# Kernel optimization log

Measured on AMD Instinct MI355X. Metric: run time of the kernel, lower is better.

The kernel has to match this reference:

```python
import jax, jax.numpy as jnp
import numpy as np

REG_CONST = 0.05  # matches init_kwargs reg_const


def setup_inputs() -> dict:
    key = jax.random.key(0)
    k1, k2, k3 = jax.random.split(key, 3)
    N, D, C = 1_000_000, 128, 10
    X_train = jax.random.normal(k1, (N, D), dtype=jnp.float32)
    y_train = jax.random.randint(k2, (N,), 0, C)
    w = jax.random.normal(k3, (C, D), dtype=jnp.float32) * 0.01
    return {"X_train": X_train, "y_train": y_train, "w": w}


def reference(X_train, y_train, w):
    """Vectorized SVM.calc_gradient: multiclass hinge loss + gradient w.r.t. w.

    Original loops over samples i and classes c:
      margin = scores[c] - scores[y_i] + 1; if margin > 0 (c != y_i):
        loss += margin; grad[y_i] += X[i]; grad[c] -= X[i]
    then loss /= N (+ 0.5*reg*||w||^2), grad /= N (+ reg*w).
    (The original seeds `gradients` with np.random.rand -- a bug; we use the
    intended zero init so the math is deterministic.)
    """
    N = X_train.shape[0]
    C = w.shape[0]
    inv_n = jnp.asarray(1.0 / N, dtype=X_train.dtype)

    scores = X_train @ w.T                                        # [N, C]
    correct = jnp.take_along_axis(scores, y_train[:, None], axis=1)  # [N, 1]
    margins = scores - correct + 1.0                              # [N, C]
    onehot = jax.nn.one_hot(y_train, C, dtype=scores.dtype)       # [N, C]
    mask = jnp.where((margins > 0) & (onehot == 0), 1.0, 0.0).astype(scores.dtype)

    loss = jnp.sum(mask * margins) * inv_n + 0.5 * REG_CONST * jnp.sum(w * w)

    # grad[c] gets -X[i] for each violating (i, c); grad[y_i] gets +X[i] per
    # violating class -> counts[i] copies of X[i] scatter-added to row y_i.
    counts = mask.sum(axis=1)                                     # [N]
    neg_part = mask.T @ X_train                                   # [C, D]
    pos_part = jax.ops.segment_sum(counts[:, None] * X_train, y_train,
                                   num_segments=C)                # [C, D]
    gradients = (pos_part - neg_part) * inv_n + REG_CONST * w
    return gradients, loss
```

## Files before the change

### kernel.cpp

```cpp
#include <hip/hip_runtime.h>

#define REG_CONST 0.05f
#define NCLASS 10
#define DIM 128
#define TILE 64
#define NBLOCKS 768
#define NTHREADS 256

__device__ __forceinline__ void async_ld16(const void* g, void* l) {
  __builtin_amdgcn_global_load_lds(
      (const __attribute__((address_space(1))) void*)g,
      (__attribute__((address_space(3))) void*)l, 16, 0, 0);
}

__global__ __launch_bounds__(NTHREADS, 3)
void svm_fused(const float* __restrict__ X, const int* __restrict__ y,
               const float* __restrict__ w, float* __restrict__ out,
               int ntiles, float inv_n) {
  __shared__ float4 xs[2048];
  __shared__ float4 coefs[192];
  __shared__ float4 wlds4[360];
  __shared__ float  lred[4];

  float* wlds = (float*)wlds4;
  const int t  = threadIdx.x;
  const int l  = t & 63;
  const int wv = t >> 6;

  for (int i = t; i < NCLASS * DIM; i += NTHREADS) {
    int d = i & 127;
    wlds[(i >> 7) * 144 + d + ((d >> 5) << 2)] = w[i];
  }

  const float4* X4 = (const float4*)X;

  const int p1row = (wv << 4) + (l >> 2);
  const int dq    = l & 3;
  const int d4p2 = t & 31;
  const int rg   = t >> 5;

  float4 g[10];
  #pragma unroll
  for (int c = 0; c < 10; ++c) g[c] = make_float4(0.f, 0.f, 0.f, 0.f);
  float loss_acc = 0.f;

  for (int tix = blockIdx.x; tix < ntiles; tix += gridDim.x) {
    const int row0 = tix * TILE;
    __syncthreads();
    #pragma unroll
    for (int ii = 0; ii < 8; ++ii) {
      int i   = (wv << 3) + ii;
      int row = (i << 1) + (l >> 5);
      int d4  = (l & 31) ^ (row & 31);
      async_ld16(X4 + (size_t)(row0 + row) * 32 + d4, xs + (i << 6) + l);
    }
    __syncthreads();

    float s[10];
    #pragma unroll
    for (int c = 0; c < 10; ++c) s[c] = 0.f;
    #pragma unroll
    for (int j = 0; j < 8; ++j) {
      int d4 = (dq << 3) + j;
      float4 x4 = xs[(p1row << 5) + (d4 ^ (p1row & 31))];
      #pragma unroll
      for (int c = 0; c < 10; ++c) {
        float4 w4 = wlds4[c * 36 + dq * 9 + j];
        s[c] = fmaf(x4.x, w4.x, fmaf(x4.y, w4.y,
               fmaf(x4.z, w4.z, fmaf(x4.w, w4.w, s[c]))));
      }
    }
    #pragma unroll
    for (int c = 0; c < 10; ++c) {
      s[c] += __shfl_xor(s[c], 1);
      s[c] += __shfl_xor(s[c], 2);
    }

    int yv = y[row0 + p1row];
    float sy = s[0];
    #pragma unroll
    for (int c = 1; c < 10; ++c) sy = (c == yv) ? s[c] : sy;

    float cnt = 0.f, rl = 0.f;
    float cf[10];
    #pragma unroll
    for (int c = 0; c < 10; ++c) {
      float m = s[c] - sy + 1.0f;
      bool act = (m > 0.f) && (c != yv);
      cf[c] = act ? -1.f : 0.f;
      cnt += act ? 1.f : 0.f;
      rl  += act ? m : 0.f;
    }
    #pragma unroll
    for (int c = 0; c < 10; ++c) cf[c] = (c == yv) ? cnt : cf[c];
    coefs[p1row * 3 + 0] = make_float4(cf[0], cf[1], cf[2], cf[3]);
    coefs[p1row * 3 + 1] = make_float4(cf[4], cf[5], cf[6], cf[7]);
    coefs[p1row * 3 + 2] = make_float4(cf[8], cf[9], 0.f, 0.f);
    if (dq == 0) loss_acc += rl;
    __syncthreads();

    #pragma unroll
    for (int k = 0; k < 8; ++k) {
      int r = (k << 3) + rg;
      float4 x4 = xs[(r << 5) + (d4p2 ^ (r & 31))];
      float4 c0 = coefs[r * 3 + 0];
      float4 c1 = coefs[r * 3 + 1];
      float4 c2 = coefs[r * 3 + 2];
#define ACC4(cc, gi)                         \
      g[gi].x = fmaf(cc, x4.x, g[gi].x);     \
      g[gi].y = fmaf(cc, x4.y, g[gi].y);     \
      g[gi].z = fmaf(cc, x4.z, g[gi].z);     \
      g[gi].w = fmaf(cc, x4.w, g[gi].w);
      ACC4(c0.x, 0) ACC4(c0.y, 1) ACC4(c0.z, 2) ACC4(c0.w, 3)
      ACC4(c1.x, 4) ACC4(c1.y, 5) ACC4(c1.z, 6) ACC4(c1.w, 7)
      ACC4(c2.x, 8) ACC4(c2.y, 9)
#undef ACC4
    }
  }

  float contrib = loss_acc * inv_n;
  if (blockIdx.x == 0) {
    float rw = 0.f;
    for (int i = t; i < NCLASS * DIM; i += NTHREADS) rw = fmaf(w[i], w[i], rw);
    contrib = fmaf(0.5f * REG_CONST, rw, contrib);
  }
  #pragma unroll
  for (int off = 32; off; off >>= 1) contrib += __shfl_down(contrib, off);
  if (l == 0) lred[wv] = contrib;
  __syncthreads();
  if (t == 0) atomicAdd(out + NCLASS * DIM, lred[0] + lred[1] + lred[2] + lred[3]);

  float4* red = xs;
  #pragma unroll
  for (int chunk = 0; chunk < 2; ++chunk) {
    __syncthreads();
    #pragma unroll
    for (int k = 0; k < 5; ++k) red[k * 256 + t] = g[chunk * 5 + k];
    __syncthreads();
    if (t < 160) {
      int k = t >> 5, dd = t & 31;
      float sx = 0.f, syy = 0.f, sz = 0.f, sw = 0.f;
      #pragma unroll
      for (int r8 = 0; r8 < 8; ++r8) {
        float4 v = red[k * 256 + (r8 << 5) + dd];
        sx += v.x; syy += v.y; sz += v.z; sw += v.w;
      }
      int c = chunk * 5 + k;
      int base = c * DIM + (dd << 2);
      float ax = sx * inv_n, ay = syy * inv_n, az = sz * inv_n, aw = sw * inv_n;
      if (blockIdx.x == 0) {
        ax += REG_CONST * w[base + 0];
        ay += REG_CONST * w[base + 1];
        az += REG_CONST * w[base + 2];
        aw += REG_CONST * w[base + 3];
      }
      atomicAdd(out + base + 0, ax);
      atomicAdd(out + base + 1, ay);
      atomicAdd(out + base + 2, az);
      atomicAdd(out + base + 3, aw);
    }
  }
}

extern "C" void kernel_launch(void* const* d_in, const int* in_sizes, int n_in,
                              void* d_out, int out_size, void* d_ws, size_t ws_size,
                              hipStream_t stream) {
  const float* X = (const float*)d_in[0];
  const int*   y = (const int*)d_in[1];
  const float* w = (const float*)d_in[2];
  float* out = (float*)d_out;
  int N = in_sizes[1];
  int ntiles = N / TILE;
  float inv_n = 1.0f / (float)N;
  hipMemsetAsync(d_out, 0, (size_t)out_size * sizeof(float), stream);
  svm_fused<<<NBLOCKS, NTHREADS, 0, stream>>>(X, y, w, out, ntiles, inv_n);
}
```

Baseline: 726.0 us.

## Double-buffer X tiles with async LDS prefetch and keep weights in registers

The kernel now double-buffers X tiles in LDS. It issues the async global-to-LDS load for the next tile before computing on the current one, which removes one block-wide barrier per tile and hides global load latency. The tile shrinks to 32 rows, and the X swizzle is dropped. Class weights now live in registers instead of LDS. Each wave handles its own 8 rows, so the per-row coefficients are shared within a wave without a barrier. The added register pressure (160 weight floats plus 40 accumulators) under launch bounds of 3 blocks per CU may cause spills.

```diff
diff --git a/kernel.cpp b/kernel.cpp
--- a/kernel.cpp
+++ b/kernel.cpp
@@ -3,7 +3,7 @@
 #define REG_CONST 0.05f
 #define NCLASS 10
 #define DIM 128
-#define TILE 64
+#define TILE 32
 #define NBLOCKS 768
 #define NTHREADS 256
 
@@ -17,55 +17,62 @@
 void svm_fused(const float* __restrict__ X, const int* __restrict__ y,
                const float* __restrict__ w, float* __restrict__ out,
                int ntiles, float inv_n) {
-  __shared__ float4 xs[2048];
-  __shared__ float4 coefs[192];
-  __shared__ float4 wlds4[360];
+  __shared__ float4 xs[2][1024];
+  __shared__ float4 coefs[96];
   __shared__ float  lred[4];
 
-  float* wlds = (float*)wlds4;
-  const int t  = threadIdx.x;
-  const int l  = t & 63;
-  const int wv = t >> 6;
+  const int t    = threadIdx.x;
+  const int l    = t & 63;
+  const int wv   = t >> 6;
+  const int dq   = l & 7;
+  const int orow = wv * 8 + (l >> 3);
+  const int d4p  = l & 31;
+  const int h    = l >> 5;
 
-  for (int i = t; i < NCLASS * DIM; i += NTHREADS) {
-    int d = i & 127;
-    wlds[(i >> 7) * 144 + d + ((d >> 5) << 2)] = w[i];
-  }
+  const float4* w4p = (const float4*)w;
+  float4 wreg[10][4];
+  #pragma unroll
+  for (int c = 0; c < 10; ++c)
+    #pragma unroll
+    for (int j = 0; j < 4; ++j)
+      wreg[c][j] = w4p[c * 32 + dq + 8 * j];
 
   const float4* X4 = (const float4*)X;
-
-  const int p1row = (wv << 4) + (l >> 2);
-  const int dq    = l & 3;
-  const int d4p2 = t & 31;
-  const int rg   = t >> 5;
 
   float4 g[10];
   #pragma unroll
   for (int c = 0; c < 10; ++c) g[c] = make_float4(0.f, 0.f, 0.f, 0.f);
   float loss_acc = 0.f;
 
-  for (int tix = blockIdx.x; tix < ntiles; tix += gridDim.x) {
-    const int row0 = tix * TILE;
+  auto stage = [&](int tix, int b) {
+    const size_t r0 = (size_t)tix * TILE;
+    #pragma unroll
+    for (int ii = 0; ii < 4; ++ii) {
+      int row = wv * 8 + ii * 2 + (l >> 5);
+      async_ld16(X4 + (r0 + row) * 32 + (l & 31),
+                 &xs[b][wv * 256 + ii * 64 + l]);
+    }
+  };
+
+  stage(blockIdx.x, 0);
+
+  int it = 0;
+  for (int tix = blockIdx.x; tix < ntiles; tix += gridDim.x, ++it) {
+    const int cur = it & 1;
     __syncthreads();
-    #pragma unroll
-    for (int ii = 0; ii < 8; ++ii) {
-      int i   = (wv << 3) + ii;
-      int row = (i << 1) + (l >> 5);
-      int d4  = (l & 31) ^ (row & 31);
-      async_ld16(X4 + (size_t)(row0 + row) * 32 + d4, xs + (i << 6) + l);
-    }
-    __syncthreads();
+    const int nxt = tix + gridDim.x;
+    if (nxt < ntiles) stage(nxt, cur ^ 1);
+    const float4* xb = xs[cur];
 
     float s[10];
     #pragma unroll
     for (int c = 0; c < 10; ++c) s[c] = 0.f;
     #pragma unroll
-    for (int j = 0; j < 8; ++j) {
-      int d4 = (dq << 3) + j;
-      float4 x4 = xs[(p1row << 5) + (d4 ^ (p1row & 31))];
+    for (int j = 0; j < 4; ++j) {
+      float4 x4 = xb[orow * 32 + dq + 8 * j];
       #pragma unroll
       for (int c = 0; c < 10; ++c) {
-        float4 w4 = wlds4[c * 36 + dq * 9 + j];
+        float4 w4 = wreg[c][j];
         s[c] = fmaf(x4.x, w4.x, fmaf(x4.y, w4.y,
                fmaf(x4.z, w4.z, fmaf(x4.w, w4.w, s[c]))));
       }
@@ -74,9 +81,10 @@
     for (int c = 0; c < 10; ++c) {
       s[c] += __shfl_xor(s[c], 1);
       s[c] += __shfl_xor(s[c], 2);
+      s[c] += __shfl_xor(s[c], 4);
     }
 
-    int yv = y[row0 + p1row];
+    int yv = y[tix * TILE + orow];
     float sy = s[0];
     #pragma unroll
     for (int c = 1; c < 10; ++c) sy = (c == yv) ? s[c] : sy;
@@ -93,16 +101,18 @@
     }
     #pragma unroll
     for (int c = 0; c < 10; ++c) cf[c] = (c == yv) ? cnt : cf[c];
-    coefs[p1row * 3 + 0] = make_float4(cf[0], cf[1], cf[2], cf[3]);
-    coefs[p1row * 3 + 1] = make_float4(cf[4], cf[5], cf[6], cf[7]);
-    coefs[p1row * 3 + 2] = make_float4(cf[8], cf[9], 0.f, 0.f);
-    if (dq == 0) loss_acc += rl;
-    __syncthreads();
+
+    if (dq == 0) {
+      coefs[orow * 3 + 0] = make_float4(cf[0], cf[1], cf[2], cf[3]);
+      coefs[orow * 3 + 1] = make_float4(cf[4], cf[5], cf[6], cf[7]);
+      coefs[orow * 3 + 2] = make_float4(cf[8], cf[9], 0.f, 0.f);
+      loss_acc += rl;
+    }
 
     #pragma unroll
-    for (int k = 0; k < 8; ++k) {
-      int r = (k << 3) + rg;
-      float4 x4 = xs[(r << 5) + (d4p2 ^ (r & 31))];
+    for (int k = 0; k < 4; ++k) {
+      int r = wv * 8 + h * 4 + k;
+      float4 x4 = xb[r * 32 + d4p];
       float4 c0 = coefs[r * 3 + 0];
       float4 c1 = coefs[r * 3 + 1];
       float4 c2 = coefs[r * 3 + 2];
@@ -130,7 +140,7 @@
   __syncthreads();
   if (t == 0) atomicAdd(out + NCLASS * DIM, lred[0] + lred[1] + lred[2] + lred[3]);
 
-  float4* red = xs;
+  float4* red = &xs[0][0];
   #pragma unroll
   for (int chunk = 0; chunk < 2; ++chunk) {
     __syncthreads();
```

Result: slower. 1.257 ms (+73.1%).
